# Kernel tuning notes

Hardware: AMD Instinct MI355X
Metric: run time of the kernel (lower is better)

Reference implementation:

```python
import jax, jax.numpy as jnp
import numpy as np

N_NODES = 100000
N_EDGES = 1600000
XN_DIM = 32
ATTR_DIM = 2 * 16 + 1  # xn_attr_dim*2 + 1 = 33


def tv_norm(x, eps=1e-3):
    x = x - jnp.mean(x, axis=1, keepdims=True)
    return x / jnp.sqrt(jnp.sum(x * x, axis=1, keepdims=True) + eps)


def setup_inputs() -> dict:
    key = jax.random.key(0)
    ks = jax.random.split(key, 7)
    xn = jax.random.normal(ks[0], (N_NODES, XN_DIM), dtype=jnp.float32)
    xe_attr = jax.random.normal(ks[1], (N_EDGES, ATTR_DIM), dtype=jnp.float32)
    # fc1: Linear(33 -> 32) with bias (stored as [in, out] for x @ W)
    W1 = jax.random.normal(ks[2], (ATTR_DIM, XN_DIM), dtype=jnp.float32) * (1.0 / np.sqrt(ATTR_DIM))
    b1 = jax.random.normal(ks[3], (XN_DIM,), dtype=jnp.float32) * 0.01
    # DoubleLayer lin1: Linear(5d -> 5d, bias=False); lin1 is applied TWICE in forward
    Wd1 = jax.random.normal(ks[4], (5 * XN_DIM, 5 * XN_DIM), dtype=jnp.float32) * (1.0 / np.sqrt(5 * XN_DIM))
    xe_src = jax.random.randint(ks[5], (N_EDGES,), 0, N_NODES, dtype=jnp.int64 if jax.config.jax_enable_x64 else jnp.int32)
    xe_dst = jax.random.randint(ks[6], (N_EDGES,), 0, N_NODES, dtype=jnp.int64 if jax.config.jax_enable_x64 else jnp.int32)
    return {"xn": xn, "xe_attr": xe_attr, "W1": W1, "b1": b1, "Wd1": Wd1,
            "xe_src": xe_src, "xe_dst": xe_dst}


def reference(xn, xe_attr, W1, b1, Wd1, xe_src, xe_dst):
    n, d = xn.shape
    # fc1: single Linear + silu activation at the end
    W = jax.nn.silu(xe_attr @ W1 + b1)               # [E, d]
    xs = xn[xe_src]                                   # gather [E, d]
    xd = xn[xe_dst]                                   # gather [E, d]
    gradX = W * (xs - xd)
    aveX = W * (xs + xd) * 0.5
    dxe = jnp.concatenate([gradX, aveX, gradX * aveX, gradX * gradX, aveX * aveX], axis=1)  # [E, 5d]
    # DoubleLayer: tanh -> lin1 -> tv_norm -> tanh -> lin1 -> tanh (lin1 used twice)
    x = jnp.tanh(dxe) @ Wd1
    x = tv_norm(x)
    x = jnp.tanh(x) @ Wd1
    dxe = jnp.tanh(x)
    msg = jnp.tile(W, (1, 5)) * dxe                   # W.repeat(1,5) * dxe
    xn_1 = jax.ops.segment_sum(msg, xe_dst, num_segments=n)  # scatter-add on dst
    xn_2 = jax.ops.segment_sum(msg, xe_src, num_segments=n)  # scatter-add on src
    xn_div = xn_1 - xn_2
    xn_ave = (xn_1 + xn_2) * 0.5
    out = (xn_div[:, :d] + xn_ave[:, d:2 * d] + xn_ave[:, 2 * d:3 * d]
           + xn_ave[:, 3 * d:4 * d] + xn_ave[:, 4 * d:])
    return out
```

## Files before the change

kernel.cpp:

```cpp
#include <hip/hip_runtime.h>
#include <cstdint>

constexpr int D      = 32;
constexpr int FD     = 160;
constexpr int ATTRD  = 33;
constexpr int WTILE  = 32;
constexpr int BLOCK  = 256;
constexpr int NKS    = 10;
constexpr int NNT    = 5;
constexpr int ASTR   = 168;
constexpr int SWSTR  = 36;
constexpr int WBYTES = 10752;

typedef __attribute__((ext_vector_type(8)))  short short8;
typedef __attribute__((ext_vector_type(16))) float f32x16;

__device__ __forceinline__ float fast_tanh(float x) {
    float e = __expf(2.0f * x);
    return 1.0f - 2.0f * __builtin_amdgcn_rcpf(e + 1.0f);
}
__device__ __forceinline__ unsigned short bf16rne(float x) {
    union { float f; unsigned u; } v; v.f = x;
    unsigned r = v.u + 0x7fffu + ((v.u >> 16) & 1u);
    return (unsigned short)(r >> 16);
}
__device__ __forceinline__ f32x16 zero16() {
    return (f32x16){0.f,0.f,0.f,0.f,0.f,0.f,0.f,0.f,0.f,0.f,0.f,0.f,0.f,0.f,0.f,0.f};
}

__global__ void prep_weights(const float* __restrict__ Wd1,
                             const float* __restrict__ W1,
                             unsigned short* __restrict__ wsb) {
    int t = blockIdx.x * blockDim.x + threadIdx.x;
    if (t < FD * FD) {
        int k = t / FD, n = t - k * FD;
        int ks = k >> 4, half = (k >> 3) & 1, j = k & 7;
        int nt = n >> 5, col = n & 31;
        int dst = ((nt * NKS + ks) * 64 + half * 32 + col) * 8 + j;
        wsb[dst] = bf16rne(Wd1[t]);
    } else if (t < FD * FD + 32 * D) {
        int t2 = t - FD * FD;
        int k = t2 >> 5, n = t2 & 31;
        int ks = k >> 4, half = (k >> 3) & 1, j = k & 7;
        int dst = FD * FD + (ks * 64 + half * 32 + n) * 8 + j;
        wsb[dst] = bf16rne(W1[k * D + n]);
    }
}

__global__ __launch_bounds__(BLOCK, 3)
void prop_mfma(const float* __restrict__ xn,
               const float* __restrict__ xe_attr,
               const float* __restrict__ W1,
               const float* __restrict__ b1,
               const unsigned short* __restrict__ wsb,
               const int*   __restrict__ esrc,
               const int*   __restrict__ edst,
               float* __restrict__ out,
               int E)
{
    __shared__ __align__(16) unsigned char sMem[4 * WBYTES];

    const int tid  = threadIdx.x;
    const int lane = tid & 63;
    const int w    = tid >> 6;
    const int col  = lane & 31;
    const int half = lane >> 5;
    unsigned char* wbase = sMem + w * WBYTES;
    float*          sW = reinterpret_cast<float*>(wbase);
    unsigned short* sA = reinterpret_cast<unsigned short*>(wbase);

    const long tile = (long)blockIdx.x * 4 + w;
    const long e0   = tile * WTILE;
    if (e0 >= (long)E) return;
    const int nv = min(WTILE, (int)((long)E - e0));

    const short8* Bp  = reinterpret_cast<const short8*>(wsb);
    const short8* W1p = reinterpret_cast<const short8*>(wsb + FD * FD);

    f32x16 Wc;
    {
        int rowA = (int)e0 + ((col < nv) ? col : 0);
        const float* ar = xe_attr + (size_t)rowA * ATTRD;
        union { short8 v; unsigned short u[8]; } A0, A1;
        #pragma unroll
        for (int j = 0; j < 8; ++j) {
            A0.u[j] = bf16rne(ar[half * 8 + j]);
            A1.u[j] = bf16rne(ar[16 + half * 8 + j]);
        }
        f32x16 c = zero16();
        c = __builtin_amdgcn_mfma_f32_32x32x16_bf16(A0.v, W1p[lane],      c, 0, 0, 0);
        c = __builtin_amdgcn_mfma_f32_32x32x16_bf16(A1.v, W1p[64 + lane], c, 0, 0, 0);

        float b1c  = b1[col];
        float w32c = W1[32 * D + col];
        #pragma unroll
        for (int r = 0; r < 16; ++r) {
            int row  = (r & 3) + 8 * (r >> 2) + 4 * half;
            int rowC = (int)e0 + ((row < nv) ? row : 0);
            float a32 = xe_attr[(size_t)rowC * ATTRD + 32];
            float x = c[r] + b1c + a32 * w32c;
            float s = x * __builtin_amdgcn_rcpf(1.0f + __expf(-x));
            Wc[r] = s;
            sW[row * SWSTR + col] = s;
        }
    }

    {
        int e  = (col < nv) ? col : 0;
        int ei = (int)e0 + e;
        int se = esrc[ei], de = edst[ei];
        const float* xsp = xn + (size_t)se * D;
        const float* xdp = xn + (size_t)de * D;
        float4 wfa = *reinterpret_cast<const float4*>(&sW[e * SWSTR + half * 8]);
        float4 wfb = *reinterpret_cast<const float4*>(&sW[e * SWSTR + half * 8 + 4]);
        float4 wfc = *reinterpret_cast<const float4*>(&sW[e * SWSTR + 16 + half * 8]);
        float4 wfd = *reinterpret_cast<const float4*>(&sW[e * SWSTR + 16 + half * 8 + 4]);
        float wf16[16] = {wfa.x,wfa.y,wfa.z,wfa.w, wfb.x,wfb.y,wfb.z,wfb.w,
                          wfc.x,wfc.y,wfc.z,wfc.w, wfd.x,wfd.y,wfd.z,wfd.w};
        #pragma unroll
        for (int p = 0; p < 2; ++p) {
            int cb = p * 16 + half * 8;
            float4 xsa = *reinterpret_cast<const float4*>(xsp + cb);
            float4 xsb = *reinterpret_cast<const float4*>(xsp + cb + 4);
            float4 xda = *reinterpret_cast<const float4*>(xdp + cb);
            float4 xdb = *reinterpret_cast<const float4*>(xdp + cb + 4);
            float xs8[8] = {xsa.x,xsa.y,xsa.z,xsa.w, xsb.x,xsb.y,xsb.z,xsb.w};
            float xd8[8] = {xda.x,xda.y,xda.z,xda.w, xdb.x,xdb.y,xdb.z,xdb.w};
            union { short8 v; unsigned short u[8]; } T[5];
            #pragma unroll
            for (int c = 0; c < 8; ++c) {
                float wfv = wf16[p * 8 + c];
                float g = wfv * (xs8[c] - xd8[c]);
                float a = wfv * (xs8[c] + xd8[c]) * 0.5f;
                T[0].u[c] = bf16rne(fast_tanh(g));
                T[1].u[c] = bf16rne(fast_tanh(a));
                T[2].u[c] = bf16rne(fast_tanh(g * a));
                T[3].u[c] = bf16rne(fast_tanh(g * g));
                T[4].u[c] = bf16rne(fast_tanh(a * a));
            }
            #pragma unroll
            for (int f = 0; f < 5; ++f)
                *reinterpret_cast<short8*>(&sA[e * ASTR + f * 32 + cb]) = T[f].v;
        }
    }

    f32x16 C[NNT];
    #pragma unroll
    for (int t = 0; t < NNT; ++t) C[t] = zero16();
    #pragma unroll
    for (int ks = 0; ks < NKS; ++ks) {
        short8 af = *reinterpret_cast<const short8*>(&sA[col * ASTR + ks * 16 + half * 8]);
        #pragma unroll
        for (int nt = 0; nt < NNT; ++nt)
            C[nt] = __builtin_amdgcn_mfma_f32_32x32x16_bf16(
                af, Bp[(nt * NKS + ks) * 64 + lane], C[nt], 0, 0, 0);
    }

    #pragma unroll
    for (int r = 0; r < 16; ++r) {
        float s = 0.f, q = 0.f;
        #pragma unroll
        for (int nt = 0; nt < NNT; ++nt) { float v = C[nt][r]; s += v; q += v * v; }
        #pragma unroll
        for (int m = 1; m < 32; m <<= 1) { s += __shfl_xor(s, m); q += __shfl_xor(q, m); }
        float mean = s * (1.0f / FD);
        float sc = __builtin_amdgcn_rsqf(q - (float)FD * mean * mean + 1e-3f);
        int row = (r & 3) + 8 * (r >> 2) + 4 * half;
        #pragma unroll
        for (int nt = 0; nt < NNT; ++nt) {
            float v = fast_tanh((C[nt][r] - mean) * sc);
            sA[row * ASTR + nt * 32 + col] = bf16rne(v);
        }
    }

    #pragma unroll
    for (int t = 0; t < NNT; ++t) C[t] = zero16();
    #pragma unroll
    for (int ks = 0; ks < NKS; ++ks) {
        short8 af = *reinterpret_cast<const short8*>(&sA[col * ASTR + ks * 16 + half * 8]);
        #pragma unroll
        for (int nt = 0; nt < NNT; ++nt)
            C[nt] = __builtin_amdgcn_mfma_f32_32x32x16_bf16(
                af, Bp[(nt * NKS + ks) * 64 + lane], C[nt], 0, 0, 0);
    }

    #pragma unroll
    for (int r = 0; r < 16; ++r) {
        int row = (r & 3) + 8 * (r >> 2) + 4 * half;
        if (row >= nv) continue;
        int sd = edst[e0 + row], ss = esrc[e0 + row];
        float wv = Wc[r];
        float m0 = fast_tanh(C[0][r]) * wv;
        float A4 = (fast_tanh(C[1][r]) + fast_tanh(C[2][r])
                  + fast_tanh(C[3][r]) + fast_tanh(C[4][r])) * wv;
        atomicAdd(out + (size_t)sd * D + col, m0 + 0.5f * A4);
        atomicAdd(out + (size_t)ss * D + col, 0.5f * A4 - m0);
    }
}

extern "C" void kernel_launch(void* const* d_in, const int* in_sizes, int n_in,
                              void* d_out, int out_size, void* d_ws, size_t ws_size,
                              hipStream_t stream)
{
    const float* xn   = (const float*)d_in[0];
    const float* attr = (const float*)d_in[1];
    const float* W1   = (const float*)d_in[2];
    const float* b1   = (const float*)d_in[3];
    const float* Wd1  = (const float*)d_in[4];
    const int*   esrc = (const int*)d_in[5];
    const int*   edst = (const int*)d_in[6];
    float* out = (float*)d_out;
    unsigned short* wsb = (unsigned short*)d_ws;

    const int E = in_sizes[5];

    hipMemsetAsync(d_out, 0, (size_t)out_size * sizeof(float), stream);
    prep_weights<<<(FD * FD + 32 * D + 255) / 256, 256, 0, stream>>>(Wd1, W1, wsb);
    const long tiles = ((long)E + WTILE - 1) / WTILE;
    const int grid = (int)((tiles + 3) / 4);
    prop_mfma<<<grid, BLOCK, 0, stream>>>(xn, attr, W1, b1, wsb, esrc, edst, out, E);
}
```

Measured before the change: 774.3 us.

## Use hardware bf16 pack, exp2 intrinsics, hoisted gathers, and shuffled indices

Replaces the software round-to-nearest bf16 conversion with the v_cvt_pk_bf16_f32 instruction and replaces __expf with direct exp2 intrinsics in tanh and silu, cutting ALU work. All global loads (attributes, edge indices, node features) are hoisted to the top of the kernel so their latency overlaps the first MFMA. Redundant global reloads of the attribute column 32 and of the edge indices in the scatter phase are replaced with lane shuffles. Keeping the hoisted values live increases register pressure, which could reduce occupancy.

```diff
diff --git a/kernel.cpp b/kernel.cpp
--- a/kernel.cpp
+++ b/kernel.cpp
@@ -15,10 +15,19 @@
 typedef __attribute__((ext_vector_type(8)))  short short8;
 typedef __attribute__((ext_vector_type(16))) float f32x16;
 
+#define TWO_LOG2E 2.8853900817779268f
+#define LOG2E     1.4426950408889634f
+
 __device__ __forceinline__ float fast_tanh(float x) {
-    float e = __expf(2.0f * x);
+    float e = __builtin_amdgcn_exp2f(x * TWO_LOG2E);
     return 1.0f - 2.0f * __builtin_amdgcn_rcpf(e + 1.0f);
 }
+__device__ __forceinline__ unsigned cvtpk(float lo, float hi) {
+    unsigned r;
+    asm("v_cvt_pk_bf16_f32 %0, %1, %2" : "=v"(r) : "v"(lo), "v"(hi));
+    return r;
+}
+
 __device__ __forceinline__ unsigned short bf16rne(float x) {
     union { float f; unsigned u; } v; v.f = x;
     unsigned r = v.u + 0x7fffu + ((v.u >> 16) & 1u);
@@ -77,15 +86,32 @@
     const short8* Bp  = reinterpret_cast<const short8*>(wsb);
     const short8* W1p = reinterpret_cast<const short8*>(wsb + FD * FD);
 
+    const int e  = (col < nv) ? col : 0;
+    const int ei = (int)e0 + e;
+    const int se = esrc[ei], de = edst[ei];
+    const float* ar  = xe_attr + (size_t)ei * ATTRD;
+    const float* xsp = xn + (size_t)se * D;
+    const float* xdp = xn + (size_t)de * D;
+    float arv0[8], arv1[8];
+    #pragma unroll
+    for (int j = 0; j < 8; ++j) { arv0[j] = ar[half * 8 + j]; arv1[j] = ar[16 + half * 8 + j]; }
+    const float a32o = ar[32];
+    float4 xs_a = *reinterpret_cast<const float4*>(xsp + half * 8);
+    float4 xs_b = *reinterpret_cast<const float4*>(xsp + half * 8 + 4);
+    float4 xs_c = *reinterpret_cast<const float4*>(xsp + 16 + half * 8);
+    float4 xs_d = *reinterpret_cast<const float4*>(xsp + 16 + half * 8 + 4);
+    float4 xd_a = *reinterpret_cast<const float4*>(xdp + half * 8);
+    float4 xd_b = *reinterpret_cast<const float4*>(xdp + half * 8 + 4);
+    float4 xd_c = *reinterpret_cast<const float4*>(xdp + 16 + half * 8);
+    float4 xd_d = *reinterpret_cast<const float4*>(xdp + 16 + half * 8 + 4);
+
     f32x16 Wc;
     {
-        int rowA = (int)e0 + ((col < nv) ? col : 0);
-        const float* ar = xe_attr + (size_t)rowA * ATTRD;
-        union { short8 v; unsigned short u[8]; } A0, A1;
-        #pragma unroll
-        for (int j = 0; j < 8; ++j) {
-            A0.u[j] = bf16rne(ar[half * 8 + j]);
-            A1.u[j] = bf16rne(ar[16 + half * 8 + j]);
+        union { unsigned u[4]; short8 v; } A0, A1;
+        #pragma unroll
+        for (int p = 0; p < 4; ++p) {
+            A0.u[p] = cvtpk(arv0[2 * p], arv0[2 * p + 1]);
+            A1.u[p] = cvtpk(arv1[2 * p], arv1[2 * p + 1]);
         }
         f32x16 c = zero16();
         c = __builtin_amdgcn_mfma_f32_32x32x16_bf16(A0.v, W1p[lane],      c, 0, 0, 0);
@@ -95,48 +121,45 @@
         float w32c = W1[32 * D + col];
         #pragma unroll
         for (int r = 0; r < 16; ++r) {
-            int row  = (r & 3) + 8 * (r >> 2) + 4 * half;
-            int rowC = (int)e0 + ((row < nv) ? row : 0);
-            float a32 = xe_attr[(size_t)rowC * ATTRD + 32];
+            int row = (r & 3) + 8 * (r >> 2) + 4 * half;
+            float a32 = __shfl(a32o, row, 32);
             float x = c[r] + b1c + a32 * w32c;
-            float s = x * __builtin_amdgcn_rcpf(1.0f + __expf(-x));
+            float s = x * __builtin_amdgcn_rcpf(1.0f + __builtin_amdgcn_exp2f(-x * LOG2E));
             Wc[r] = s;
             sW[row * SWSTR + col] = s;
         }
     }
 
     {
-        int e  = (col < nv) ? col : 0;
-        int ei = (int)e0 + e;
-        int se = esrc[ei], de = edst[ei];
-        const float* xsp = xn + (size_t)se * D;
-        const float* xdp = xn + (size_t)de * D;
         float4 wfa = *reinterpret_cast<const float4*>(&sW[e * SWSTR + half * 8]);
         float4 wfb = *reinterpret_cast<const float4*>(&sW[e * SWSTR + half * 8 + 4]);
         float4 wfc = *reinterpret_cast<const float4*>(&sW[e * SWSTR + 16 + half * 8]);
         float4 wfd = *reinterpret_cast<const float4*>(&sW[e * SWSTR + 16 + half * 8 + 4]);
         float wf16[16] = {wfa.x,wfa.y,wfa.z,wfa.w, wfb.x,wfb.y,wfb.z,wfb.w,
                           wfc.x,wfc.y,wfc.z,wfc.w, wfd.x,wfd.y,wfd.z,wfd.w};
+        float xs16[16] = {xs_a.x,xs_a.y,xs_a.z,xs_a.w, xs_b.x,xs_b.y,xs_b.z,xs_b.w,
+                          xs_c.x,xs_c.y,xs_c.z,xs_c.w, xs_d.x,xs_d.y,xs_d.z,xs_d.w};
+        float xd16[16] = {xd_a.x,xd_a.y,xd_a.z,xd_a.w, xd_b.x,xd_b.y,xd_b.z,xd_b.w,
+                          xd_c.x,xd_c.y,xd_c.z,xd_c.w, xd_d.x,xd_d.y,xd_d.z,xd_d.w};
         #pragma unroll
         for (int p = 0; p < 2; ++p) {
             int cb = p * 16 + half * 8;
-            float4 xsa = *reinterpret_cast<const float4*>(xsp + cb);
-            float4 xsb = *reinterpret_cast<const float4*>(xsp + cb + 4);
-            float4 xda = *reinterpret_cast<const float4*>(xdp + cb);
-            float4 xdb = *reinterpret_cast<const float4*>(xdp + cb + 4);
-            float xs8[8] = {xsa.x,xsa.y,xsa.z,xsa.w, xsb.x,xsb.y,xsb.z,xsb.w};
-            float xd8[8] = {xda.x,xda.y,xda.z,xda.w, xdb.x,xdb.y,xdb.z,xdb.w};
-            union { short8 v; unsigned short u[8]; } T[5];
+            float g8[8], a8[8];
             #pragma unroll
             for (int c = 0; c < 8; ++c) {
                 float wfv = wf16[p * 8 + c];
-                float g = wfv * (xs8[c] - xd8[c]);
-                float a = wfv * (xs8[c] + xd8[c]) * 0.5f;
-                T[0].u[c] = bf16rne(fast_tanh(g));
-                T[1].u[c] = bf16rne(fast_tanh(a));
-                T[2].u[c] = bf16rne(fast_tanh(g * a));
-                T[3].u[c] = bf16rne(fast_tanh(g * g));
-                T[4].u[c] = bf16rne(fast_tanh(a * a));
+                g8[c] = wfv * (xs16[p * 8 + c] - xd16[p * 8 + c]);
+                a8[c] = wfv * (xs16[p * 8 + c] + xd16[p * 8 + c]) * 0.5f;
+            }
+            union { unsigned u[4]; short8 v; } T[5];
+            #pragma unroll
+            for (int q = 0; q < 4; ++q) {
+                int c0 = 2 * q, c1 = 2 * q + 1;
+                T[0].u[q] = cvtpk(fast_tanh(g8[c0]),         fast_tanh(g8[c1]));
+                T[1].u[q] = cvtpk(fast_tanh(a8[c0]),         fast_tanh(a8[c1]));
+                T[2].u[q] = cvtpk(fast_tanh(g8[c0]*a8[c0]),  fast_tanh(g8[c1]*a8[c1]));
+                T[3].u[q] = cvtpk(fast_tanh(g8[c0]*g8[c0]),  fast_tanh(g8[c1]*g8[c1]));
+                T[4].u[q] = cvtpk(fast_tanh(a8[c0]*a8[c0]),  fast_tanh(a8[c1]*a8[c1]));
             }
             #pragma unroll
             for (int f = 0; f < 5; ++f)
@@ -166,11 +189,19 @@
         float mean = s * (1.0f / FD);
         float sc = __builtin_amdgcn_rsqf(q - (float)FD * mean * mean + 1e-3f);
         int row = (r & 3) + 8 * (r >> 2) + 4 * half;
-        #pragma unroll
-        for (int nt = 0; nt < NNT; ++nt) {
-            float v = fast_tanh((C[nt][r] - mean) * sc);
-            sA[row * ASTR + nt * 32 + col] = bf16rne(v);
-        }
+        float t0 = fast_tanh((C[0][r] - mean) * sc);
+        float t1 = fast_tanh((C[1][r] - mean) * sc);
+        float t2 = fast_tanh((C[2][r] - mean) * sc);
+        float t3 = fast_tanh((C[3][r] - mean) * sc);
+        float t4 = fast_tanh((C[4][r] - mean) * sc);
+        unsigned p01 = cvtpk(t0, t1);
+        unsigned p23 = cvtpk(t2, t3);
+        unsigned p4  = cvtpk(t4, t4);
+        sA[row * ASTR +   0 + col] = (unsigned short)p01;
+        sA[row * ASTR +  32 + col] = (unsigned short)(p01 >> 16);
+        sA[row * ASTR +  64 + col] = (unsigned short)p23;
+        sA[row * ASTR +  96 + col] = (unsigned short)(p23 >> 16);
+        sA[row * ASTR + 128 + col] = (unsigned short)p4;
     }
 
     #pragma unroll
@@ -188,7 +219,8 @@
     for (int r = 0; r < 16; ++r) {
         int row = (r & 3) + 8 * (r >> 2) + 4 * half;
         if (row >= nv) continue;
-        int sd = edst[e0 + row], ss = esrc[e0 + row];
+        int sd = __shfl(de, row, 32);
+        int ss = __shfl(se, row, 32);
         float wv = Wc[r];
         float m0 = fast_tanh(C[0][r]) * wv;
         float A4 = (fast_tanh(C[1][r]) + fast_tanh(C[2][r])
```

Measured after the change: 919.8 us. 18.8% more time.
